# Optimization experiments

Hardware: AMD Instinct MI355X
Metric: run time of the kernel (lower is better)

Reference implementation:

```python
import jax, jax.numpy as jnp
import numpy as np

N_NODES = 50000
IN_CH = 256
N_REL = 5
N_EDGES = 800000
LAST_SENSES = 25000
LAST_GLOBALS = 45000


def setup_inputs() -> dict:
    key = jax.random.key(0)
    ks = jax.random.split(key, 12)
    batch_x = jax.random.normal(ks[0], (N_NODES, IN_CH), dtype=jnp.float32)
    batch_edge_index = jax.random.randint(ks[1], (2, N_EDGES), 0, N_NODES)
    batch_edge_type = jax.random.randint(ks[2], (N_EDGES,), 0, N_REL)
    s = 1.0 / np.sqrt(IN_CH)
    comp = jax.random.normal(ks[3], (N_REL, N_REL), dtype=jnp.float32) * (1.0 / np.sqrt(N_REL))
    basis = jax.random.normal(ks[4], (N_REL, IN_CH, IN_CH), dtype=jnp.float32) * s
    root = jax.random.normal(ks[5], (IN_CH, IN_CH), dtype=jnp.float32) * s
    bias = jnp.zeros((IN_CH,), dtype=jnp.float32)
    n_glob = LAST_GLOBALS - LAST_SENSES
    Wg = jax.random.normal(ks[6], (n_glob, IN_CH), dtype=jnp.float32) * s
    bg = jnp.zeros((n_glob,), dtype=jnp.float32)
    Ws = jax.random.normal(ks[7], (LAST_SENSES, IN_CH), dtype=jnp.float32) * s
    bs = jnp.zeros((LAST_SENSES,), dtype=jnp.float32)
    return {
        'batch_x': batch_x,
        'batch_edge_index': batch_edge_index,
        'batch_edge_type': batch_edge_type,
        'comp': comp,
        'basis': basis,
        'root': root,
        'bias': bias,
        'Wg': Wg,
        'bg': bg,
        'Ws': Ws,
        'bs': bs,
    }


def _rgcn_conv(x, edge_index, edge_type, comp, basis, root, bias):
    # Basis decomposition: W_r = sum_b comp[r,b] * basis[b]  -> [R, d, d]
    R = comp.shape[0]
    N = x.shape[0]
    W = jnp.einsum('rb,bdf->rdf', comp, basis)
    # Transform all nodes by every relation weight once ([R,N,F]), then gather
    # per edge instead of doing an [E,d,d] weight gather.
    H = jnp.einsum('nd,rdf->rnf', x, W)
    src, dst = edge_index[0], edge_index[1]
    msgs = H[edge_type, src]                     # [E, F]
    seg = edge_type * N + dst                    # combined (relation, dst) id
    sums = jax.ops.segment_sum(msgs, seg, num_segments=R * N)
    cnt = jax.ops.segment_sum(jnp.ones((msgs.shape[0],), msgs.dtype), seg,
                              num_segments=R * N)
    mean = sums / jnp.maximum(cnt, 1.0)[:, None]  # per-relation mean aggregation
    agg = mean.reshape(R, N, -1).sum(axis=0)
    return agg + x @ root + bias


def reference(batch_x, batch_edge_index, batch_edge_type, comp, basis, root,
              bias, Wg, bg, Ws, bs):
    h = jax.nn.relu(_rgcn_conv(batch_x, batch_edge_index, batch_edge_type,
                               comp, basis, root, bias))
    x1 = h[0]                                    # current node embedding [F]
    logits_global = Wg @ x1 + bg
    logits_sense = Ws @ x1 + bs
    return (jax.nn.log_softmax(logits_global, axis=0),
            jax.nn.log_softmax(logits_sense, axis=0))
```

## Files before the change

### kernel.cpp

```cpp
#include <hip/hip_runtime.h>
#include <math.h>

#define N_NODES 50000
#define IN_CH 256
#define N_REL 5
#define N_EDGES 800000
#define N_E4 200000
#define N_GLOB 20000
#define N_SENSE 25000
#define N_OUT 45000
#define MAX_MATCH 256
#define N_QUAD 11250
#define Q_GLOB 5000

#define G2 1024
#define G3 2048

#define WS_SUMS 327680
#define WS_ROOTACC 328960
#define WS_IP 329216
#define WS_PM 329744

__device__ __forceinline__ void omerge(float& m, float& s, float m2, float s2) {
    float M = fmaxf(m, m2);
    if (M == -INFINITY) return;
    s = s * expf(m - M) + s2 * expf(m2 - M);
    m = M;
}

__device__ __forceinline__ void rec(const int* __restrict__ ei,
                                    const int* __restrict__ et,
                                    int* __restrict__ ip, int e) {
    int t = et[e];
    int p = atomicAdd(&ip[0], 1);
    if (p < MAX_MATCH) {
        ip[8 + p] = ei[e];
        ip[8 + MAX_MATCH + p] = t;
    }
    atomicAdd(&ip[1 + t], 1);
}

__global__ __launch_bounds__(256) void k1(const float* __restrict__ x,
                                          const int* __restrict__ ei,
                                          const int* __restrict__ et,
                                          const float* __restrict__ comp,
                                          const float* __restrict__ basis,
                                          const float* __restrict__ root,
                                          float* __restrict__ base) {
    float* W = base;
    float* rootacc = base + WS_ROOTACC;
    int* ip = (int*)(base + WS_IP);
    int bid = blockIdx.x, tid = threadIdx.x;
    if (bid < 1280) {
        int idx = bid * 256 + tid;
        int r = idx >> 16, df = idx & 65535;
        float acc = 0.f;
#pragma unroll
        for (int b = 0; b < N_REL; ++b)
            acc += comp[r * N_REL + b] * basis[b * (IN_CH * IN_CH) + df];
        W[idx] = acc;
    } else if (bid < 2062) {
        int e4 = (bid - 1280) * 256 + tid;
        if (e4 < N_E4) {
            int4 d = ((const int4*)(ei + N_EDGES))[e4];
            int e = e4 * 4;
            if (d.x == 0) rec(ei, et, ip, e);
            if (d.y == 0) rec(ei, et, ip, e + 1);
            if (d.z == 0) rec(ei, et, ip, e + 2);
            if (d.w == 0) rec(ei, et, ip, e + 3);
        }
    } else {
        int c = bid - 2062;
        const float* xp = x + c * 64;
        const float* rp = root + c * 64 * IN_CH + tid;
        float acc = 0.f;
#pragma unroll 8
        for (int d = 0; d < 64; ++d) acc += xp[d] * rp[d * IN_CH];
        atomicAdd(&rootacc[tid], acc);
    }
}

__global__ __launch_bounds__(256) void k2(const float* __restrict__ x,
                                          float* __restrict__ base) {
    const float* W = base;
    float* sums = base + WS_SUMS;
    const int* ip = (const int*)(base + WS_IP);
    int tid = threadIdx.x, bid = blockIdx.x;

    int m = ip[0]; if (m > MAX_MATCH) m = MAX_MATCH;
    if (bid >= 4 * m) return;
    int j = bid >> 2, c = bid & 3;
    int s = ip[8 + j];
    int r = ip[8 + MAX_MATCH + j];
    const float* xp = x + (size_t)s * IN_CH + c * 64;
    const float* wp = W + r * (IN_CH * IN_CH) + c * 64 * IN_CH + tid;
    float acc = 0.f;
#pragma unroll 8
    for (int d = 0; d < 64; ++d) acc += xp[d] * wp[d * IN_CH];
    atomicAdd(&sums[r * IN_CH + tid], acc);
}

__global__ __launch_bounds__(256) void k3(const float* __restrict__ bias,
                                          const float* __restrict__ Wg,
                                          const float* __restrict__ bg,
                                          const float* __restrict__ Ws,
                                          const float* __restrict__ bs,
                                          float* __restrict__ out,
                                          float* __restrict__ base) {
    __shared__ float rbuf[4][4];
    const float* sums = base + WS_SUMS;
    const float* rootacc = base + WS_ROOTACC;
    const int* ip = (const int*)(base + WS_IP);
    float* pm_g = base + WS_PM;
    float* ps_g = pm_g + G3;
    float* pm_s = ps_g + G3;
    float* ps_s = pm_s + G3;

    int tid = threadIdx.x, bid = blockIdx.x;
    const int lane = tid & 63, w = tid >> 6;

    float4 xv;
    {
        float4 bq = ((const float4*)bias)[lane];
        float4 ra = ((const float4*)rootacc)[lane];
        xv.x = bq.x + ra.x; xv.y = bq.y + ra.y;
        xv.z = bq.z + ra.z; xv.w = bq.w + ra.w;
#pragma unroll
        for (int r = 0; r < N_REL; ++r) {
            float4 sv = ((const float4*)(sums + r * IN_CH))[lane];
            float inv = 1.f / fmaxf((float)ip[1 + r], 1.f);
            xv.x += sv.x * inv; xv.y += sv.y * inv;
            xv.z += sv.z * inv; xv.w += sv.w * inv;
        }
        xv.x = fmaxf(xv.x, 0.f); xv.y = fmaxf(xv.y, 0.f);
        xv.z = fmaxf(xv.z, 0.f); xv.w = fmaxf(xv.w, 0.f);
    }

    float mg = -INFINITY, sg = 0.f, ms = -INFINITY, ss = 0.f;

    for (int q = bid * 4 + w; q < N_QUAD; q += G3 * 4) {
        const float* mat; const float* bv; int rl;
        if (q < Q_GLOB) { mat = Wg; bv = bg; rl = q * 4; }
        else            { mat = Ws; bv = bs; rl = q * 4 - N_GLOB; }
        const float4* p = (const float4*)(mat + (size_t)rl * IN_CH);
        float4 a0 = p[lane], a1 = p[64 + lane], a2 = p[128 + lane], a3 = p[192 + lane];
        float d0 = a0.x * xv.x + a0.y * xv.y + a0.z * xv.z + a0.w * xv.w;
        float d1 = a1.x * xv.x + a1.y * xv.y + a1.z * xv.z + a1.w * xv.w;
        float d2 = a2.x * xv.x + a2.y * xv.y + a2.z * xv.z + a2.w * xv.w;
        float d3 = a3.x * xv.x + a3.y * xv.y + a3.z * xv.z + a3.w * xv.w;
#pragma unroll
        for (int off = 32; off; off >>= 1) {
            d0 += __shfl_xor(d0, off); d1 += __shfl_xor(d1, off);
            d2 += __shfl_xor(d2, off); d3 += __shfl_xor(d3, off);
        }
        float4 bq = *(const float4*)(bv + rl);
        float l0 = d0 + bq.x, l1 = d1 + bq.y, l2 = d2 + bq.z, l3 = d3 + bq.w;
        if (lane == 0) ((float4*)out)[q] = make_float4(l0, l1, l2, l3);
        float lm = fmaxf(fmaxf(l0, l1), fmaxf(l2, l3));
        float le = expf(l0 - lm) + expf(l1 - lm) + expf(l2 - lm) + expf(l3 - lm);
        if (q < Q_GLOB) omerge(mg, sg, lm, le);
        else            omerge(ms, ss, lm, le);
    }
    if (lane == 0) { rbuf[w][0] = mg; rbuf[w][1] = sg; rbuf[w][2] = ms; rbuf[w][3] = ss; }
    __syncthreads();
    if (tid == 0) {
        float M0 = rbuf[0][0], S0 = rbuf[0][1], M1 = rbuf[0][2], S1 = rbuf[0][3];
#pragma unroll
        for (int i = 1; i < 4; ++i) {
            omerge(M0, S0, rbuf[i][0], rbuf[i][1]);
            omerge(M1, S1, rbuf[i][2], rbuf[i][3]);
        }
        pm_g[bid] = M0; ps_g[bid] = S0; pm_s[bid] = M1; ps_s[bid] = S1;
    }
}

__global__ __launch_bounds__(256) void k4(float* __restrict__ out,
                                          const float* __restrict__ base) {
    __shared__ float rm[256], rs[256];
    const float* pm_g = base + WS_PM;
    const float* ps_g = pm_g + G3;
    const float* pm_s = ps_g + G3;
    const float* ps_s = pm_s + G3;
    int tid = threadIdx.x;
    int i = blockIdx.x * 256 + tid;
    float v = (i < N_OUT) ? out[i] : 0.f;

    float M = -INFINITY, S = 0.f;
#pragma unroll
    for (int j = 0; j < G3 / 256; ++j) omerge(M, S, pm_g[tid + j * 256], ps_g[tid + j * 256]);
    rm[tid] = M; rs[tid] = S; __syncthreads();
    for (int h = 128; h; h >>= 1) {
        if (tid < h) omerge(rm[tid], rs[tid], rm[tid + h], rs[tid + h]);
        __syncthreads();
    }
    float zg = rm[0] + logf(rs[0]);
    __syncthreads();

    M = -INFINITY; S = 0.f;
#pragma unroll
    for (int j = 0; j < G3 / 256; ++j) omerge(M, S, pm_s[tid + j * 256], ps_s[tid + j * 256]);
    rm[tid] = M; rs[tid] = S; __syncthreads();
    for (int h = 128; h; h >>= 1) {
        if (tid < h) omerge(rm[tid], rs[tid], rm[tid + h], rs[tid + h]);
        __syncthreads();
    }
    float zs = rm[0] + logf(rs[0]);

    if (i < N_OUT) out[i] = v - ((i < N_GLOB) ? zg : zs);
}

extern "C" void kernel_launch(void* const* d_in, const int* in_sizes, int n_in,
                              void* d_out, int out_size, void* d_ws, size_t ws_size,
                              hipStream_t stream) {
    const float* x     = (const float*)d_in[0];
    const int*   ei    = (const int*)  d_in[1];
    const int*   et    = (const int*)  d_in[2];
    const float* comp  = (const float*)d_in[3];
    const float* basis = (const float*)d_in[4];
    const float* root  = (const float*)d_in[5];
    const float* bias  = (const float*)d_in[6];
    const float* Wg    = (const float*)d_in[7];
    const float* bg    = (const float*)d_in[8];
    const float* Wsn   = (const float*)d_in[9];
    const float* bs    = (const float*)d_in[10];
    float* out  = (float*)d_out;
    float* base = (float*)d_ws;

    hipMemsetAsync(base + WS_SUMS, 0, 6176, stream);

    k1<<<2066, 256, 0, stream>>>(x, ei, et, comp, basis, root, base);
    k2<<<G2,   256, 0, stream>>>(x, base);
    k3<<<G3,   256, 0, stream>>>(bias, Wg, bg, Wsn, bs, out, base);
    k4<<<(N_OUT + 255) / 256, 256, 0, stream>>>(out, base);
}
```

Baseline: 146.6 us.

## Aggregate source rows per relation before applying basis weights

Node 0's incoming source features are summed per relation with atomics while scanning edges. Then comp coefficients and inverse counts are folded into a per-basis vector, which is multiplied once by each basis matrix. This drops the dense 5x256x256 W construction and the per-edge matvec kernel, reordering the maths by linearity. The cost is many float atomics per matched edge in the scan kernel, and it also removes the match-count cap.

```diff
diff --git a/kernel.cpp b/kernel.cpp
--- a/kernel.cpp
+++ b/kernel.cpp
@@ -9,17 +9,14 @@
 #define N_GLOB 20000
 #define N_SENSE 25000
 #define N_OUT 45000
-#define MAX_MATCH 256
 #define N_QUAD 11250
 #define Q_GLOB 5000
-
-#define G2 1024
 #define G3 2048
 
-#define WS_SUMS 327680
-#define WS_ROOTACC 328960
-#define WS_IP 329216
-#define WS_PM 329744
+#define WS_XSUM 0
+#define WS_CNT 1280
+#define WS_AGG 1288
+#define WS_PM 2048
 
 __device__ __forceinline__ void omerge(float& m, float& s, float m2, float s2) {
     float M = fmaxf(m, m2);
@@ -28,89 +25,77 @@
     m = M;
 }
 
-__device__ __forceinline__ void rec(const int* __restrict__ ei,
-                                    const int* __restrict__ et,
-                                    int* __restrict__ ip, int e) {
-    int t = et[e];
-    int p = atomicAdd(&ip[0], 1);
-    if (p < MAX_MATCH) {
-        ip[8 + p] = ei[e];
-        ip[8 + MAX_MATCH + p] = t;
-    }
-    atomicAdd(&ip[1 + t], 1);
-}
-
-__global__ __launch_bounds__(256) void k1(const float* __restrict__ x,
-                                          const int* __restrict__ ei,
-                                          const int* __restrict__ et,
-                                          const float* __restrict__ comp,
-                                          const float* __restrict__ basis,
-                                          const float* __restrict__ root,
-                                          float* __restrict__ base) {
-    float* W = base;
-    float* rootacc = base + WS_ROOTACC;
-    int* ip = (int*)(base + WS_IP);
+__global__ __launch_bounds__(256) void k_scan(const float* __restrict__ x,
+                                              const int* __restrict__ ei,
+                                              const int* __restrict__ et,
+                                              float* __restrict__ base) {
+    float* xsum = base + WS_XSUM;
+    float* cntf = base + WS_CNT;
+    int e4 = blockIdx.x * 256 + threadIdx.x;
+    if (e4 >= N_E4) return;
+    int4 d = ((const int4*)(ei + N_EDGES))[e4];
+    int e = e4 * 4;
+    for (int k = 0; k < 4; ++k) {
+        int dk = (k == 0) ? d.x : (k == 1) ? d.y : (k == 2) ? d.z : d.w;
+        if (dk == 0) {
+            int t = et[e + k];
+            atomicAdd(&cntf[t], 1.0f);
+            const float4* xr = (const float4*)(x + (size_t)ei[e + k] * IN_CH);
+            float* xs = xsum + t * IN_CH;
+#pragma unroll 1
+            for (int i = 0; i < 64; ++i) {
+                float4 v = xr[i];
+                atomicAdd(&xs[i * 4 + 0], v.x); atomicAdd(&xs[i * 4 + 1], v.y);
+                atomicAdd(&xs[i * 4 + 2], v.z); atomicAdd(&xs[i * 4 + 3], v.w);
+            }
+        }
+    }
+}
+
+__global__ __launch_bounds__(256) void k_agg(const float* __restrict__ x,
+                                             const float* __restrict__ comp,
+                                             const float* __restrict__ basis,
+                                             const float* __restrict__ root,
+                                             float* __restrict__ base) {
+    __shared__ float vlds[64];
+    const float* xsum = base + WS_XSUM;
+    const float* cntf = base + WS_CNT;
+    float* agg = base + WS_AGG;
     int bid = blockIdx.x, tid = threadIdx.x;
-    if (bid < 1280) {
-        int idx = bid * 256 + tid;
-        int r = idx >> 16, df = idx & 65535;
-        float acc = 0.f;
-#pragma unroll
-        for (int b = 0; b < N_REL; ++b)
-            acc += comp[r * N_REL + b] * basis[b * (IN_CH * IN_CH) + df];
-        W[idx] = acc;
-    } else if (bid < 2062) {
-        int e4 = (bid - 1280) * 256 + tid;
-        if (e4 < N_E4) {
-            int4 d = ((const int4*)(ei + N_EDGES))[e4];
-            int e = e4 * 4;
-            if (d.x == 0) rec(ei, et, ip, e);
-            if (d.y == 0) rec(ei, et, ip, e + 1);
-            if (d.z == 0) rec(ei, et, ip, e + 2);
-            if (d.w == 0) rec(ei, et, ip, e + 3);
-        }
+    float acc = 0.f;
+    if (bid < 20) {
+        int b = bid >> 2, c = bid & 3;
+        if (tid < 64) {
+            int dg = c * 64 + tid;
+            float v = 0.f;
+#pragma unroll
+            for (int r = 0; r < N_REL; ++r)
+                v += comp[r * N_REL + b] * xsum[r * IN_CH + dg] / fmaxf(cntf[r], 1.f);
+            vlds[tid] = v;
+        }
+        __syncthreads();
+        const float* bp = basis + b * (IN_CH * IN_CH) + c * 64 * IN_CH + tid;
+#pragma unroll 8
+        for (int dd = 0; dd < 64; ++dd) acc += vlds[dd] * bp[dd * IN_CH];
     } else {
-        int c = bid - 2062;
+        int c = bid - 20;
         const float* xp = x + c * 64;
         const float* rp = root + c * 64 * IN_CH + tid;
-        float acc = 0.f;
 #pragma unroll 8
-        for (int d = 0; d < 64; ++d) acc += xp[d] * rp[d * IN_CH];
-        atomicAdd(&rootacc[tid], acc);
-    }
-}
-
-__global__ __launch_bounds__(256) void k2(const float* __restrict__ x,
-                                          float* __restrict__ base) {
-    const float* W = base;
-    float* sums = base + WS_SUMS;
-    const int* ip = (const int*)(base + WS_IP);
-    int tid = threadIdx.x, bid = blockIdx.x;
-
-    int m = ip[0]; if (m > MAX_MATCH) m = MAX_MATCH;
-    if (bid >= 4 * m) return;
-    int j = bid >> 2, c = bid & 3;
-    int s = ip[8 + j];
-    int r = ip[8 + MAX_MATCH + j];
-    const float* xp = x + (size_t)s * IN_CH + c * 64;
-    const float* wp = W + r * (IN_CH * IN_CH) + c * 64 * IN_CH + tid;
-    float acc = 0.f;
-#pragma unroll 8
-    for (int d = 0; d < 64; ++d) acc += xp[d] * wp[d * IN_CH];
-    atomicAdd(&sums[r * IN_CH + tid], acc);
-}
-
-__global__ __launch_bounds__(256) void k3(const float* __restrict__ bias,
-                                          const float* __restrict__ Wg,
-                                          const float* __restrict__ bg,
-                                          const float* __restrict__ Ws,
-                                          const float* __restrict__ bs,
-                                          float* __restrict__ out,
-                                          float* __restrict__ base) {
+        for (int dd = 0; dd < 64; ++dd) acc += xp[dd] * rp[dd * IN_CH];
+    }
+    atomicAdd(&agg[tid], acc);
+}
+
+__global__ __launch_bounds__(256) void k_logits(const float* __restrict__ bias,
+                                                const float* __restrict__ Wg,
+                                                const float* __restrict__ bg,
+                                                const float* __restrict__ Ws,
+                                                const float* __restrict__ bs,
+                                                float* __restrict__ out,
+                                                float* __restrict__ base) {
     __shared__ float rbuf[4][4];
-    const float* sums = base + WS_SUMS;
-    const float* rootacc = base + WS_ROOTACC;
-    const int* ip = (const int*)(base + WS_IP);
+    const float* agg = base + WS_AGG;
     float* pm_g = base + WS_PM;
     float* ps_g = pm_g + G3;
     float* pm_s = ps_g + G3;
@@ -122,18 +107,9 @@
     float4 xv;
     {
         float4 bq = ((const float4*)bias)[lane];
-        float4 ra = ((const float4*)rootacc)[lane];
-        xv.x = bq.x + ra.x; xv.y = bq.y + ra.y;
-        xv.z = bq.z + ra.z; xv.w = bq.w + ra.w;
-#pragma unroll
-        for (int r = 0; r < N_REL; ++r) {
-            float4 sv = ((const float4*)(sums + r * IN_CH))[lane];
-            float inv = 1.f / fmaxf((float)ip[1 + r], 1.f);
-            xv.x += sv.x * inv; xv.y += sv.y * inv;
-            xv.z += sv.z * inv; xv.w += sv.w * inv;
-        }
-        xv.x = fmaxf(xv.x, 0.f); xv.y = fmaxf(xv.y, 0.f);
-        xv.z = fmaxf(xv.z, 0.f); xv.w = fmaxf(xv.w, 0.f);
+        float4 aq = ((const float4*)agg)[lane];
+        xv.x = fmaxf(bq.x + aq.x, 0.f); xv.y = fmaxf(bq.y + aq.y, 0.f);
+        xv.z = fmaxf(bq.z + aq.z, 0.f); xv.w = fmaxf(bq.w + aq.w, 0.f);
     }
 
     float mg = -INFINITY, sg = 0.f, ms = -INFINITY, ss = 0.f;
@@ -174,8 +150,8 @@
     }
 }
 
-__global__ __launch_bounds__(256) void k4(float* __restrict__ out,
-                                          const float* __restrict__ base) {
+__global__ __launch_bounds__(256) void k_norm(float* __restrict__ out,
+                                              const float* __restrict__ base) {
     __shared__ float rm[256], rs[256];
     const float* pm_g = base + WS_PM;
     const float* ps_g = pm_g + G3;
@@ -226,10 +202,10 @@
     float* out  = (float*)d_out;
     float* base = (float*)d_ws;
 
-    hipMemsetAsync(base + WS_SUMS, 0, 6176, stream);
-
-    k1<<<2066, 256, 0, stream>>>(x, ei, et, comp, basis, root, base);
-    k2<<<G2,   256, 0, stream>>>(x, base);
-    k3<<<G3,   256, 0, stream>>>(bias, Wg, bg, Wsn, bs, out, base);
-    k4<<<(N_OUT + 255) / 256, 256, 0, stream>>>(out, base);
-}
+    hipMemsetAsync(base, 0, 6176, stream);
+
+    k_scan  <<<(N_E4 + 255) / 256, 256, 0, stream>>>(x, ei, et, base);
+    k_agg   <<<24, 256, 0, stream>>>(x, comp, basis, root, base);
+    k_logits<<<G3, 256, 0, stream>>>(bias, Wg, bg, Wsn, bs, out, base);
+    k_norm  <<<(N_OUT + 255) / 256, 256, 0, stream>>>(out, base);
+}
```

Measured after the change: 168.5 us. +15.0%, slower.
